# Performance work log

Measured on AMD Instinct MI355X. Metric: run time of the kernel, lower is better.

Reference implementation:

```python
import jax, jax.numpy as jnp
import numpy as np
from jax import lax

S = 2                      # window half-size (matches init_kwargs s)
K = 2 * S + 1              # kernel size = 5
SZ = float(K ** 3)         # number of voxels in the window
EPS = 1e-10


def _box_sum(x):
    """Replicate-pad then valid 3D box-sum with an all-ones K^3 kernel.
    x: [N, 1, D, H, W] -> [N, 1, D, H, W]. Same math as F.pad(mode='replicate')
    followed by Conv3d(ones kernel, valid)."""
    xp = jnp.pad(x, ((0, 0), (0, 0), (S, S), (S, S), (S, S)), mode='edge')
    kern = jnp.ones((1, 1, K, K, K), dtype=x.dtype)
    return lax.conv_general_dilated(
        xp, kern, window_strides=(1, 1, 1), padding='VALID',
        dimension_numbers=('NCDHW', 'OIDHW', 'NCDHW'))


def setup_inputs() -> dict:
    key = jax.random.key(0)
    k1, k2 = jax.random.split(key)
    shape = (2, 1, 160, 160, 160)
    im_fixed = jax.random.normal(k1, shape, dtype=jnp.float32)
    im_moving = jax.random.normal(k2, shape, dtype=jnp.float32)
    mask = jnp.ones(shape, dtype=jnp.float32)
    return {"im_fixed": im_fixed, "im_moving": im_moving, "mask": mask}


def reference(im_fixed, im_moving, mask):
    # local means
    u_F = _box_sum(im_fixed) / SZ
    u_M = _box_sum(im_moving) / SZ
    # local variances (box-sum of squared centered values, then / SZ)
    sigma_F = jnp.sqrt(_box_sum((im_fixed - u_F) ** 2) / SZ)
    sigma_M = jnp.sqrt(_box_sum((im_moving - u_M) ** 2) / SZ)
    # normalized images
    n_F = (im_fixed - u_F) / (sigma_F + EPS)
    n_M = (im_moving - u_M) / (sigma_M + EPS)
    # local cross-correlation map (box-sum, NOT divided by SZ, as in torch code)
    cross = _box_sum(n_F * n_M)
    # reduce: negative masked sum of squared LCC
    return -1.0 * jnp.sum(cross ** 2 * mask)
```

## Files before the change

### kernel.cpp

```cpp
#include <hip/hip_runtime.h>

namespace {

constexpr int LEN   = 160;
constexpr int PLANE = LEN * LEN;
constexpr int VOL   = LEN * PLANE;
constexpr float INV_SZ = 1.0f / 125.0f;
constexpr float EPS_   = 1e-10f;

constexpr int TX = 32, TY = 32, ZC = 16;
constexpr int RX = TX + 4, RY = TY + 4;
constexpr int NRAW = RX * RY;
constexpr int NCHZ = LEN / ZC;
constexpr int NBX = LEN / TX, NBY = LEN / TY;
constexpr int NXY = NBX * NBY;
constexpr int BLK  = 512;
constexpr int NWG  = NBX * NBY * NCHZ * 2;
constexpr int QW   = NWG / 8, RW = NWG % 8;

__device__ __forceinline__ int clampi(int v) {
  return v < 0 ? 0 : (v > LEN - 1 ? LEN - 1 : v);
}

struct BlkInfo { int x0, y0, z0; size_t base; };
__device__ __forceinline__ BlkInfo decodeBlock() {
  const int g = blockIdx.x + NBX * (blockIdx.y + NBY * blockIdx.z);
  const int xcd = g & 7, idx = g >> 3;
  const int w = (xcd < RW) ? xcd * (QW + 1) + idx
                           : RW * (QW + 1) + (xcd - RW) * QW + idx;
  const int half = NWG / 2;
  const int batch = w / half;
  const int rem   = w % half;
  const int zc = rem / NXY, tl = rem % NXY;
  BlkInfo bi;
  bi.x0 = (tl % NBX) * TX;
  bi.y0 = (tl / NBX) * TY;
  bi.z0 = zc * ZC;
  bi.base = (size_t)batch * VOL;
  return bi;
}

__global__ __launch_bounds__(BLK) void fuseAB(const float* __restrict__ inA,
                                              const float* __restrict__ inB,
                                              float* __restrict__ outP) {
  __shared__ __align__(16) float raw[2][2][RY][RX];
  __shared__ __align__(16) float xs [4][2][RY][RX];

  const int tid = threadIdx.x;
  const BlkInfo bi = decodeBlock();
  const int x0 = bi.x0, y0 = bi.y0, z0 = bi.z0;
  const size_t base = bi.base;

  int off[3], lly[3], llx[3];
  bool act[3];
#pragma unroll
  for (int j = 0; j < 3; ++j) {
    int i = tid + j * BLK;
    act[j] = i < NRAW;
    int ii = act[j] ? i : 0;
    lly[j] = ii / RX; llx[j] = ii % RX;
    off[j] = clampi(y0 - 2 + lly[j]) * LEN + clampi(x0 - 2 + llx[j]);
  }

  const int ly  = tid >> 4;
  const int lx0 = (tid & 15) * 2;

  float pA[2][3], pB[2][3];
  float2 rzF[6], rzM[6], rzF2[6], rzM2[6];
  float2 cnF[4], cnM[4];

  auto loadPair = [&](int t) {
#pragma unroll
    for (int p = 0; p < 2; ++p) {
      const size_t pb = base + (size_t)clampi(t + p) * PLANE;
#pragma unroll
      for (int j = 0; j < 3; ++j)
        if (act[j]) { pA[p][j] = inA[pb + off[j]]; pB[p][j] = inB[pb + off[j]]; }
    }
  };
  auto depositPair = [&]() {
#pragma unroll
    for (int p = 0; p < 2; ++p)
#pragma unroll
      for (int j = 0; j < 3; ++j)
        if (act[j]) {
          raw[0][p][lly[j]][llx[j]] = pA[p][j];
          raw[1][p][lly[j]][llx[j]] = pB[p][j];
        }
  };

  auto xsumTask = [&](int tt) {
    const int f = tt & 1, c = (tt >> 1) & 7, r = tt >> 4;
#pragma unroll
    for (int p = 0; p < 2; ++p) {
      const float* rp = &raw[f][p][r][4 * c];
      const float4 u = *(const float4*)rp;
      const float4 v = *(const float4*)(rp + 4);
      const float m = u.y + u.z + u.w;
      float4 s;
      s.x = m + u.x + v.x;
      s.y = m + v.x + v.y;
      s.z = s.y - u.y + v.z;
      s.w = s.z - u.z + v.w;
      *(float4*)&xs[f][p][r][4 * c] = s;
      float4 uq, vq;
      uq.x = u.x * u.x; uq.y = u.y * u.y; uq.z = u.z * u.z; uq.w = u.w * u.w;
      vq.x = v.x * v.x; vq.y = v.y * v.y; vq.z = v.z * v.z; vq.w = v.w * v.w;
      const float mq = uq.y + uq.z + uq.w;
      float4 q;
      q.x = mq + uq.x + vq.x;
      q.y = mq + vq.x + vq.y;
      q.z = q.y - uq.y + vq.z;
      q.w = q.z - uq.z + vq.w;
      *(float4*)&xs[2 + f][p][r][4 * c] = q;
    }
  };

  loadPair(z0 - 2);
  depositPair();
  __syncthreads();

  for (int t = z0 - 2; t <= z0 + ZC; t += 2) {
    if (t + 2 <= z0 + ZC) loadPair(t + 2);

    xsumTask(tid);
    if (tid < 576 - BLK) xsumTask(tid + BLK);

    cnF[0] = cnF[2]; cnF[1] = cnF[3]; cnM[0] = cnM[2]; cnM[1] = cnM[3];
    cnF[2] = *(const float2*)&raw[0][0][ly + 2][lx0 + 2];
    cnF[3] = *(const float2*)&raw[0][1][ly + 2][lx0 + 2];
    cnM[2] = *(const float2*)&raw[1][0][ly + 2][lx0 + 2];
    cnM[3] = *(const float2*)&raw[1][1][ly + 2][lx0 + 2];

    __syncthreads();

    if (t + 2 <= z0 + ZC) depositPair();

#pragma unroll
    for (int s = 0; s < 4; ++s) {
      rzF[s] = rzF[s + 2]; rzM[s] = rzM[s + 2];
      rzF2[s] = rzF2[s + 2]; rzM2[s] = rzM2[s + 2];
    }
#pragma unroll
    for (int p = 0; p < 2; ++p) {
      float2 sf = {0.f, 0.f}, sm = {0.f, 0.f};
      float2 sf2 = {0.f, 0.f}, sm2 = {0.f, 0.f};
#pragma unroll
      for (int k = 0; k < 5; ++k) {
        const float2 a  = *(const float2*)&xs[0][p][ly + k][lx0];
        const float2 b  = *(const float2*)&xs[1][p][ly + k][lx0];
        const float2 a2 = *(const float2*)&xs[2][p][ly + k][lx0];
        const float2 b2 = *(const float2*)&xs[3][p][ly + k][lx0];
        sf.x += a.x;  sf.y += a.y;  sm.x += b.x;  sm.y += b.y;
        sf2.x += a2.x; sf2.y += a2.y; sm2.x += b2.x; sm2.y += b2.y;
      }
      rzF[4 + p] = sf; rzM[4 + p] = sm;
      rzF2[4 + p] = sf2; rzM2[4 + p] = sm2;
    }

    if (t >= z0 + 2) {
#pragma unroll
      for (int q = 0; q < 2; ++q) {
        const int zo = t - 2 + q;
        float2 bF = {0.f, 0.f}, bM = {0.f, 0.f};
        float2 bF2 = {0.f, 0.f}, bM2 = {0.f, 0.f};
#pragma unroll
        for (int s = 0; s < 5; ++s) {
          bF.x += rzF[q + s].x;  bF.y += rzF[q + s].y;
          bM.x += rzM[q + s].x;  bM.y += rzM[q + s].y;
          bF2.x += rzF2[q + s].x; bF2.y += rzF2[q + s].y;
          bM2.x += rzM2[q + s].x; bM2.y += rzM2[q + s].y;
        }
        const size_t g = base + (size_t)zo * PLANE + (size_t)(y0 + ly) * LEN + (x0 + lx0);
        float2 o;
        {
          const float uF = bF.x * INV_SZ, uM = bM.x * INV_SZ;
          const float vF = fmaxf(bF2.x * INV_SZ - uF * uF, 0.f);
          const float vM = fmaxf(bM2.x * INV_SZ - uM * uM, 0.f);
          o.x = ((cnF[q].x - uF) / (sqrtf(vF) + EPS_)) *
                ((cnM[q].x - uM) / (sqrtf(vM) + EPS_));
        }
        {
          const float uF = bF.y * INV_SZ, uM = bM.y * INV_SZ;
          const float vF = fmaxf(bF2.y * INV_SZ - uF * uF, 0.f);
          const float vM = fmaxf(bM2.y * INV_SZ - uM * uM, 0.f);
          o.y = ((cnF[q].y - uF) / (sqrtf(vF) + EPS_)) *
                ((cnM[q].y - uM) / (sqrtf(vM) + EPS_));
        }
        *(float2*)&outP[g] = o;
      }
    }
    __syncthreads();
  }
}

__global__ __launch_bounds__(BLK) void slab1_reduce(const float* __restrict__ p,
                                                    const float* __restrict__ mask,
                                                    float* __restrict__ out) {
  __shared__ __align__(16) float raw[2][RY][RX];
  __shared__ __align__(16) float xs [2][RY][RX];
  __shared__ float wsum[BLK / 64];

  const int tid = threadIdx.x;
  const BlkInfo bi = decodeBlock();
  const int x0 = bi.x0, y0 = bi.y0, z0 = bi.z0;
  const size_t base = bi.base;

  int off[3], lly[3], llx[3];
  bool act[3];
#pragma unroll
  for (int j = 0; j < 3; ++j) {
    int i = tid + j * BLK;
    act[j] = i < NRAW;
    int ii = act[j] ? i : 0;
    lly[j] = ii / RX; llx[j] = ii % RX;
    off[j] = clampi(y0 - 2 + lly[j]) * LEN + clampi(x0 - 2 + llx[j]);
  }
  const int ly  = tid >> 4;
  const int lx0 = (tid & 15) * 2;

  float pf[2][3];
  float2 rz[6];
  float acc = 0.f;

  auto loadPair = [&](int t) {
#pragma unroll
    for (int pp = 0; pp < 2; ++pp) {
      const size_t pb = base + (size_t)clampi(t + pp) * PLANE;
#pragma unroll
      for (int j = 0; j < 3; ++j)
        if (act[j]) pf[pp][j] = p[pb + off[j]];
    }
  };
  auto depositPair = [&]() {
#pragma unroll
    for (int pp = 0; pp < 2; ++pp)
#pragma unroll
      for (int j = 0; j < 3; ++j)
        if (act[j]) raw[pp][lly[j]][llx[j]] = pf[pp][j];
  };

  loadPair(z0 - 2);
  depositPair();
  __syncthreads();

  for (int t = z0 - 2; t <= z0 + ZC; t += 2) {
    if (t + 2 <= z0 + ZC) loadPair(t + 2);

    if (tid < 288) {
      const int c = tid & 7, r = tid >> 3;
#pragma unroll
      for (int pp = 0; pp < 2; ++pp) {
        const float* rp = &raw[pp][r][4 * c];
        const float4 u = *(const float4*)rp;
        const float4 v = *(const float4*)(rp + 4);
        const float m = u.y + u.z + u.w;
        float4 s;
        s.x = m + u.x + v.x;
        s.y = m + v.x + v.y;
        s.z = s.y - u.y + v.z;
        s.w = s.z - u.z + v.w;
        *(float4*)&xs[pp][r][4 * c] = s;
      }
    }
    __syncthreads();

    if (t + 2 <= z0 + ZC) depositPair();

#pragma unroll
    for (int s = 0; s < 4; ++s) rz[s] = rz[s + 2];
#pragma unroll
    for (int pp = 0; pp < 2; ++pp) {
      float2 s2 = {0.f, 0.f};
#pragma unroll
      for (int k = 0; k < 5; ++k) {
        const float2 a = *(const float2*)&xs[pp][ly + k][lx0];
        s2.x += a.x; s2.y += a.y;
      }
      rz[4 + pp] = s2;
    }

    if (t >= z0 + 2) {
#pragma unroll
      for (int q = 0; q < 2; ++q) {
        const int zo = t - 2 + q;
        float2 bs = {0.f, 0.f};
#pragma unroll
        for (int s = 0; s < 5; ++s) { bs.x += rz[q + s].x; bs.y += rz[q + s].y; }
        const size_t g = base + (size_t)zo * PLANE + (size_t)(y0 + ly) * LEN + (x0 + lx0);
        const float2 mk = *(const float2*)&mask[g];
        acc += bs.x * bs.x * mk.x + bs.y * bs.y * mk.y;
      }
    }
    __syncthreads();
  }

#pragma unroll
  for (int o = 32; o > 0; o >>= 1) acc += __shfl_down(acc, o, 64);
  const int lane = tid & 63, wid = tid >> 6;
  if (lane == 0) wsum[wid] = acc;
  __syncthreads();
  if (tid == 0) {
    float t = 0.f;
#pragma unroll
    for (int w = 0; w < BLK / 64; ++w) t += wsum[w];
    atomicAdd(out, -t);
  }
}

}

extern "C" void kernel_launch(void* const* d_in, const int* in_sizes, int n_in,
                              void* d_out, int out_size, void* d_ws, size_t ws_size,
                              hipStream_t stream) {
  const float* F    = (const float*)d_in[0];
  const float* M    = (const float*)d_in[1];
  const float* mask = (const float*)d_in[2];
  float* out = (float*)d_out;

  float* pB = (float*)d_ws;

  hipMemsetAsync(d_out, 0, sizeof(float), stream);

  dim3 grd(NBX, NBY, NCHZ * 2), blk(BLK);

  fuseAB<<<grd, blk, 0, stream>>>(F, M, pB);
  slab1_reduce<<<grd, blk, 0, stream>>>(pB, mask, out);
}
```

Before: 186.4 us.

## Shrink tiles to 32x16 with one voxel per thread and precomputed LDS pointers

Halves the y tile height so each 512-thread block covers 32x16 voxels, one per thread, instead of two. The grid doubles, which gives more blocks to spread over the CUs. Shared-memory x-sum buffers drop their halo columns, and the per-thread addresses for LDS deposits and x-sum tasks are computed once before the loop. The smaller tile raises the halo overhead in y (20 staged rows for 16 outputs instead of 36 for 32) and narrows global stores from float2 to scalar. The XCD remap is hardcoded to the new block count of 1000.

```diff
diff --git a/kernel.cpp b/kernel.cpp
--- a/kernel.cpp
+++ b/kernel.cpp
@@ -8,15 +8,13 @@
 constexpr float INV_SZ = 1.0f / 125.0f;
 constexpr float EPS_   = 1e-10f;
 
-constexpr int TX = 32, TY = 32, ZC = 16;
+constexpr int TX = 32, TY = 16, ZC = 16;
 constexpr int RX = TX + 4, RY = TY + 4;
 constexpr int NRAW = RX * RY;
 constexpr int NCHZ = LEN / ZC;
 constexpr int NBX = LEN / TX, NBY = LEN / TY;
 constexpr int NXY = NBX * NBY;
 constexpr int BLK  = 512;
-constexpr int NWG  = NBX * NBY * NCHZ * 2;
-constexpr int QW   = NWG / 8, RW = NWG % 8;
 
 __device__ __forceinline__ int clampi(int v) {
   return v < 0 ? 0 : (v > LEN - 1 ? LEN - 1 : v);
@@ -25,10 +23,8 @@
 struct BlkInfo { int x0, y0, z0; size_t base; };
 __device__ __forceinline__ BlkInfo decodeBlock() {
   const int g = blockIdx.x + NBX * (blockIdx.y + NBY * blockIdx.z);
-  const int xcd = g & 7, idx = g >> 3;
-  const int w = (xcd < RW) ? xcd * (QW + 1) + idx
-                           : RW * (QW + 1) + (xcd - RW) * QW + idx;
-  const int half = NWG / 2;
+  const int w = (g & 7) * 125 + (g >> 3);
+  const int half = NXY * NCHZ;
   const int batch = w / half;
   const int rem   = w % half;
   const int zc = rem / NXY, tl = rem % NXY;
@@ -44,37 +40,57 @@
                                               const float* __restrict__ inB,
                                               float* __restrict__ outP) {
   __shared__ __align__(16) float raw[2][2][RY][RX];
-  __shared__ __align__(16) float xs [4][2][RY][RX];
+  __shared__ __align__(16) float xs [4][2][RY][TX];
 
   const int tid = threadIdx.x;
   const BlkInfo bi = decodeBlock();
   const int x0 = bi.x0, y0 = bi.y0, z0 = bi.z0;
   const size_t base = bi.base;
 
-  int off[3], lly[3], llx[3];
-  bool act[3];
-#pragma unroll
-  for (int j = 0; j < 3; ++j) {
+  int off[2]; float* ldst[2][2][2];
+  bool act[2];
+#pragma unroll
+  for (int j = 0; j < 2; ++j) {
     int i = tid + j * BLK;
     act[j] = i < NRAW;
     int ii = act[j] ? i : 0;
-    lly[j] = ii / RX; llx[j] = ii % RX;
-    off[j] = clampi(y0 - 2 + lly[j]) * LEN + clampi(x0 - 2 + llx[j]);
-  }
-
-  const int ly  = tid >> 4;
-  const int lx0 = (tid & 15) * 2;
-
-  float pA[2][3], pB[2][3];
-  float2 rzF[6], rzM[6], rzF2[6], rzM2[6];
-  float2 cnF[4], cnM[4];
+    const int ry = ii / RX, rx = ii % RX;
+    off[j] = clampi(y0 - 2 + ry) * LEN + clampi(x0 - 2 + rx);
+#pragma unroll
+    for (int f = 0; f < 2; ++f)
+#pragma unroll
+      for (int p = 0; p < 2; ++p) ldst[j][f][p] = &raw[f][p][ry][rx];
+  }
+
+  const float* tsrc[2]; float* tdst[2]; int ntask = (tid < 128) ? 2 : 1;
+#pragma unroll
+  for (int k = 0; k < 2; ++k) {
+    int tt = (k == 0) ? tid : tid + BLK;
+    if (tt >= 640) tt = 0;
+    const int p = tt / 320, r1 = tt % 320;
+    const int f = r1 / 160, r2 = r1 % 160;
+    const int r = r2 / 8,  c = r2 % 8;
+    tsrc[k] = &raw[f][p][r][4 * c];
+    tdst[k] = &xs[f][p][r][4 * c];
+  }
+  if (tid >= 128) ntask = 1;
+
+  const int ly = tid >> 5, lx = tid & 31;
+  const int sOff = (y0 + ly) * LEN + (x0 + lx);
+  const float* ybase = &xs[0][0][ly][lx];
+  constexpr int AS = 2 * RY * TX;
+  constexpr int PS = RY * TX;
+
+  float pA[2][2], pB[2][2];
+  float rzF[6], rzM[6], rzF2[6], rzM2[6];
+  float cnF[4], cnM[4];
 
   auto loadPair = [&](int t) {
 #pragma unroll
     for (int p = 0; p < 2; ++p) {
       const size_t pb = base + (size_t)clampi(t + p) * PLANE;
 #pragma unroll
-      for (int j = 0; j < 3; ++j)
+      for (int j = 0; j < 2; ++j)
         if (act[j]) { pA[p][j] = inA[pb + off[j]]; pB[p][j] = inB[pb + off[j]]; }
     }
   };
@@ -82,214 +98,195 @@
 #pragma unroll
     for (int p = 0; p < 2; ++p)
 #pragma unroll
-      for (int j = 0; j < 3; ++j)
-        if (act[j]) {
-          raw[0][p][lly[j]][llx[j]] = pA[p][j];
-          raw[1][p][lly[j]][llx[j]] = pB[p][j];
+      for (int j = 0; j < 2; ++j)
+        if (act[j]) { *ldst[j][0][p] = pA[p][j]; *ldst[j][1][p] = pB[p][j]; }
+  };
+
+  auto xsumTask = [&](int k) {
+    const float4 u = *(const float4*)tsrc[k];
+    const float4 v = *(const float4*)(tsrc[k] + 4);
+    const float m = u.y + u.z + u.w;
+    float4 s;
+    s.x = m + u.x + v.x;
+    s.y = m + v.x + v.y;
+    s.z = s.y - u.y + v.z;
+    s.w = s.z - u.z + v.w;
+    *(float4*)tdst[k] = s;
+    float4 uq, vq;
+    uq.x = u.x * u.x; uq.y = u.y * u.y; uq.z = u.z * u.z; uq.w = u.w * u.w;
+    vq.x = v.x * v.x; vq.y = v.y * v.y; vq.z = v.z * v.z; vq.w = v.w * v.w;
+    const float mq = uq.y + uq.z + uq.w;
+    float4 q;
+    q.x = mq + uq.x + vq.x;
+    q.y = mq + vq.x + vq.y;
+    q.z = q.y - uq.y + vq.z;
+    q.w = q.z - uq.z + vq.w;
+    *(float4*)(tdst[k] + 2 * AS) = q;
+  };
+
+  loadPair(z0 - 2);
+  depositPair();
+  __syncthreads();
+
+  for (int t = z0 - 2; t <= z0 + ZC; t += 2) {
+    if (t + 2 <= z0 + ZC) loadPair(t + 2);
+
+    xsumTask(0);
+    if (ntask == 2) xsumTask(1);
+
+    cnF[0] = cnF[2]; cnF[1] = cnF[3]; cnM[0] = cnM[2]; cnM[1] = cnM[3];
+    cnF[2] = raw[0][0][ly + 2][lx + 2];
+    cnF[3] = raw[0][1][ly + 2][lx + 2];
+    cnM[2] = raw[1][0][ly + 2][lx + 2];
+    cnM[3] = raw[1][1][ly + 2][lx + 2];
+
+    __syncthreads();
+
+    if (t + 2 <= z0 + ZC) depositPair();
+
+#pragma unroll
+    for (int s = 0; s < 4; ++s) {
+      rzF[s] = rzF[s + 2]; rzM[s] = rzM[s + 2];
+      rzF2[s] = rzF2[s + 2]; rzM2[s] = rzM2[s + 2];
+    }
+#pragma unroll
+    for (int p = 0; p < 2; ++p) {
+      float sf = 0.f, sm = 0.f, sf2 = 0.f, sm2 = 0.f;
+#pragma unroll
+      for (int k = 0; k < 5; ++k) {
+        sf  += ybase[0 * AS + p * PS + k * TX];
+        sm  += ybase[1 * AS + p * PS + k * TX];
+        sf2 += ybase[2 * AS + p * PS + k * TX];
+        sm2 += ybase[3 * AS + p * PS + k * TX];
+      }
+      rzF[4 + p] = sf; rzM[4 + p] = sm;
+      rzF2[4 + p] = sf2; rzM2[4 + p] = sm2;
+    }
+
+    if (t >= z0 + 2) {
+#pragma unroll
+      for (int q = 0; q < 2; ++q) {
+        const int zo = t - 2 + q;
+        float bF = 0.f, bM = 0.f, bF2 = 0.f, bM2 = 0.f;
+#pragma unroll
+        for (int s = 0; s < 5; ++s) {
+          bF += rzF[q + s]; bM += rzM[q + s];
+          bF2 += rzF2[q + s]; bM2 += rzM2[q + s];
         }
-  };
-
-  auto xsumTask = [&](int tt) {
-    const int f = tt & 1, c = (tt >> 1) & 7, r = tt >> 4;
-#pragma unroll
-    for (int p = 0; p < 2; ++p) {
-      const float* rp = &raw[f][p][r][4 * c];
-      const float4 u = *(const float4*)rp;
-      const float4 v = *(const float4*)(rp + 4);
+        const float uF = bF * INV_SZ, uM = bM * INV_SZ;
+        const float vF = fmaxf(bF2 * INV_SZ - uF * uF, 0.f);
+        const float vM = fmaxf(bM2 * INV_SZ - uM * uM, 0.f);
+        const float o = ((cnF[q] - uF) / (sqrtf(vF) + EPS_)) *
+                        ((cnM[q] - uM) / (sqrtf(vM) + EPS_));
+        outP[base + (size_t)zo * PLANE + sOff] = o;
+      }
+    }
+    __syncthreads();
+  }
+}
+
+__global__ __launch_bounds__(BLK) void slab1_reduce(const float* __restrict__ p,
+                                                    const float* __restrict__ mask,
+                                                    float* __restrict__ out) {
+  __shared__ __align__(16) float raw[2][RY][RX];
+  __shared__ __align__(16) float xs [2][RY][TX];
+  __shared__ float wsum[BLK / 64];
+
+  const int tid = threadIdx.x;
+  const BlkInfo bi = decodeBlock();
+  const int x0 = bi.x0, y0 = bi.y0, z0 = bi.z0;
+  const size_t base = bi.base;
+
+  int off[2]; float* ldst[2][2];
+  bool act[2];
+#pragma unroll
+  for (int j = 0; j < 2; ++j) {
+    int i = tid + j * BLK;
+    act[j] = i < NRAW;
+    int ii = act[j] ? i : 0;
+    const int ry = ii / RX, rx = ii % RX;
+    off[j] = clampi(y0 - 2 + ry) * LEN + clampi(x0 - 2 + rx);
+#pragma unroll
+    for (int pp = 0; pp < 2; ++pp) ldst[j][pp] = &raw[pp][ry][rx];
+  }
+
+  const bool tact = tid < 320;
+  const float* tsrc; float* tdst;
+  {
+    int tt = tact ? tid : 0;
+    const int pp = tt / 160, r1 = tt % 160;
+    const int r = r1 / 8, c = r1 % 8;
+    tsrc = &raw[pp][r][4 * c];
+    tdst = &xs[pp][r][4 * c];
+  }
+
+  const int ly = tid >> 5, lx = tid & 31;
+  const int sOff = (y0 + ly) * LEN + (x0 + lx);
+  const float* ybase = &xs[0][ly][lx];
+  constexpr int PS = RY * TX;
+
+  float pf[2][2];
+  float rz[6];
+  float acc = 0.f;
+
+  auto loadPair = [&](int t) {
+#pragma unroll
+    for (int pp = 0; pp < 2; ++pp) {
+      const size_t pb = base + (size_t)clampi(t + pp) * PLANE;
+#pragma unroll
+      for (int j = 0; j < 2; ++j)
+        if (act[j]) pf[pp][j] = p[pb + off[j]];
+    }
+  };
+  auto depositPair = [&]() {
+#pragma unroll
+    for (int pp = 0; pp < 2; ++pp)
+#pragma unroll
+      for (int j = 0; j < 2; ++j)
+        if (act[j]) *ldst[j][pp] = pf[pp][j];
+  };
+
+  loadPair(z0 - 2);
+  depositPair();
+  __syncthreads();
+
+  for (int t = z0 - 2; t <= z0 + ZC; t += 2) {
+    if (t + 2 <= z0 + ZC) loadPair(t + 2);
+
+    if (tact) {
+      const float4 u = *(const float4*)tsrc;
+      const float4 v = *(const float4*)(tsrc + 4);
       const float m = u.y + u.z + u.w;
       float4 s;
       s.x = m + u.x + v.x;
       s.y = m + v.x + v.y;
       s.z = s.y - u.y + v.z;
       s.w = s.z - u.z + v.w;
-      *(float4*)&xs[f][p][r][4 * c] = s;
-      float4 uq, vq;
-      uq.x = u.x * u.x; uq.y = u.y * u.y; uq.z = u.z * u.z; uq.w = u.w * u.w;
-      vq.x = v.x * v.x; vq.y = v.y * v.y; vq.z = v.z * v.z; vq.w = v.w * v.w;
-      const float mq = uq.y + uq.z + uq.w;
-      float4 q;
-      q.x = mq + uq.x + vq.x;
-      q.y = mq + vq.x + vq.y;
-      q.z = q.y - uq.y + vq.z;
-      q.w = q.z - uq.z + vq.w;
-      *(float4*)&xs[2 + f][p][r][4 * c] = q;
-    }
-  };
-
-  loadPair(z0 - 2);
-  depositPair();
-  __syncthreads();
-
-  for (int t = z0 - 2; t <= z0 + ZC; t += 2) {
-    if (t + 2 <= z0 + ZC) loadPair(t + 2);
-
-    xsumTask(tid);
-    if (tid < 576 - BLK) xsumTask(tid + BLK);
-
-    cnF[0] = cnF[2]; cnF[1] = cnF[3]; cnM[0] = cnM[2]; cnM[1] = cnM[3];
-    cnF[2] = *(const float2*)&raw[0][0][ly + 2][lx0 + 2];
-    cnF[3] = *(const float2*)&raw[0][1][ly + 2][lx0 + 2];
-    cnM[2] = *(const float2*)&raw[1][0][ly + 2][lx0 + 2];
-    cnM[3] = *(const float2*)&raw[1][1][ly + 2][lx0 + 2];
-
+      *(float4*)tdst = s;
+    }
     __syncthreads();
 
     if (t + 2 <= z0 + ZC) depositPair();
 
 #pragma unroll
-    for (int s = 0; s < 4; ++s) {
-      rzF[s] = rzF[s + 2]; rzM[s] = rzM[s + 2];
-      rzF2[s] = rzF2[s + 2]; rzM2[s] = rzM2[s + 2];
-    }
-#pragma unroll
-    for (int p = 0; p < 2; ++p) {
-      float2 sf = {0.f, 0.f}, sm = {0.f, 0.f};
-      float2 sf2 = {0.f, 0.f}, sm2 = {0.f, 0.f};
-#pragma unroll
-      for (int k = 0; k < 5; ++k) {
-        const float2 a  = *(const float2*)&xs[0][p][ly + k][lx0];
-        const float2 b  = *(const float2*)&xs[1][p][ly + k][lx0];
-        const float2 a2 = *(const float2*)&xs[2][p][ly + k][lx0];
-        const float2 b2 = *(const float2*)&xs[3][p][ly + k][lx0];
-        sf.x += a.x;  sf.y += a.y;  sm.x += b.x;  sm.y += b.y;
-        sf2.x += a2.x; sf2.y += a2.y; sm2.x += b2.x; sm2.y += b2.y;
-      }
-      rzF[4 + p] = sf; rzM[4 + p] = sm;
-      rzF2[4 + p] = sf2; rzM2[4 + p] = sm2;
+    for (int s = 0; s < 4; ++s) rz[s] = rz[s + 2];
+#pragma unroll
+    for (int pp = 0; pp < 2; ++pp) {
+      float s2 = 0.f;
+#pragma unroll
+      for (int k = 0; k < 5; ++k) s2 += ybase[pp * PS + k * TX];
+      rz[4 + pp] = s2;
     }
 
     if (t >= z0 + 2) {
 #pragma unroll
       for (int q = 0; q < 2; ++q) {
         const int zo = t - 2 + q;
-        float2 bF = {0.f, 0.f}, bM = {0.f, 0.f};
-        float2 bF2 = {0.f, 0.f}, bM2 = {0.f, 0.f};
-#pragma unroll
-        for (int s = 0; s < 5; ++s) {
-          bF.x += rzF[q + s].x;  bF.y += rzF[q + s].y;
-          bM.x += rzM[q + s].x;  bM.y += rzM[q + s].y;
-          bF2.x += rzF2[q + s].x; bF2.y += rzF2[q + s].y;
-          bM2.x += rzM2[q + s].x; bM2.y += rzM2[q + s].y;
-        }
-        const size_t g = base + (size_t)zo * PLANE + (size_t)(y0 + ly) * LEN + (x0 + lx0);
-        float2 o;
-        {
-          const float uF = bF.x * INV_SZ, uM = bM.x * INV_SZ;
-          const float vF = fmaxf(bF2.x * INV_SZ - uF * uF, 0.f);
-          const float vM = fmaxf(bM2.x * INV_SZ - uM * uM, 0.f);
-          o.x = ((cnF[q].x - uF) / (sqrtf(vF) + EPS_)) *
-                ((cnM[q].x - uM) / (sqrtf(vM) + EPS_));
-        }
-        {
-          const float uF = bF.y * INV_SZ, uM = bM.y * INV_SZ;
-          const float vF = fmaxf(bF2.y * INV_SZ - uF * uF, 0.f);
-          const float vM = fmaxf(bM2.y * INV_SZ - uM * uM, 0.f);
-          o.y = ((cnF[q].y - uF) / (sqrtf(vF) + EPS_)) *
-                ((cnM[q].y - uM) / (sqrtf(vM) + EPS_));
-        }
-        *(float2*)&outP[g] = o;
-      }
-    }
-    __syncthreads();
-  }
-}
-
-__global__ __launch_bounds__(BLK) void slab1_reduce(const float* __restrict__ p,
-                                                    const float* __restrict__ mask,
-                                                    float* __restrict__ out) {
-  __shared__ __align__(16) float raw[2][RY][RX];
-  __shared__ __align__(16) float xs [2][RY][RX];
-  __shared__ float wsum[BLK / 64];
-
-  const int tid = threadIdx.x;
-  const BlkInfo bi = decodeBlock();
-  const int x0 = bi.x0, y0 = bi.y0, z0 = bi.z0;
-  const size_t base = bi.base;
-
-  int off[3], lly[3], llx[3];
-  bool act[3];
-#pragma unroll
-  for (int j = 0; j < 3; ++j) {
-    int i = tid + j * BLK;
-    act[j] = i < NRAW;
-    int ii = act[j] ? i : 0;
-    lly[j] = ii / RX; llx[j] = ii % RX;
-    off[j] = clampi(y0 - 2 + lly[j]) * LEN + clampi(x0 - 2 + llx[j]);
-  }
-  const int ly  = tid >> 4;
-  const int lx0 = (tid & 15) * 2;
-
-  float pf[2][3];
-  float2 rz[6];
-  float acc = 0.f;
-
-  auto loadPair = [&](int t) {
-#pragma unroll
-    for (int pp = 0; pp < 2; ++pp) {
-      const size_t pb = base + (size_t)clampi(t + pp) * PLANE;
-#pragma unroll
-      for (int j = 0; j < 3; ++j)
-        if (act[j]) pf[pp][j] = p[pb + off[j]];
-    }
-  };
-  auto depositPair = [&]() {
-#pragma unroll
-    for (int pp = 0; pp < 2; ++pp)
-#pragma unroll
-      for (int j = 0; j < 3; ++j)
-        if (act[j]) raw[pp][lly[j]][llx[j]] = pf[pp][j];
-  };
-
-  loadPair(z0 - 2);
-  depositPair();
-  __syncthreads();
-
-  for (int t = z0 - 2; t <= z0 + ZC; t += 2) {
-    if (t + 2 <= z0 + ZC) loadPair(t + 2);
-
-    if (tid < 288) {
-      const int c = tid & 7, r = tid >> 3;
-#pragma unroll
-      for (int pp = 0; pp < 2; ++pp) {
-        const float* rp = &raw[pp][r][4 * c];
-        const float4 u = *(const float4*)rp;
-        const float4 v = *(const float4*)(rp + 4);
-        const float m = u.y + u.z + u.w;
-        float4 s;
-        s.x = m + u.x + v.x;
-        s.y = m + v.x + v.y;
-        s.z = s.y - u.y + v.z;
-        s.w = s.z - u.z + v.w;
-        *(float4*)&xs[pp][r][4 * c] = s;
-      }
-    }
-    __syncthreads();
-
-    if (t + 2 <= z0 + ZC) depositPair();
-
-#pragma unroll
-    for (int s = 0; s < 4; ++s) rz[s] = rz[s + 2];
-#pragma unroll
-    for (int pp = 0; pp < 2; ++pp) {
-      float2 s2 = {0.f, 0.f};
-#pragma unroll
-      for (int k = 0; k < 5; ++k) {
-        const float2 a = *(const float2*)&xs[pp][ly + k][lx0];
-        s2.x += a.x; s2.y += a.y;
-      }
-      rz[4 + pp] = s2;
-    }
-
-    if (t >= z0 + 2) {
-#pragma unroll
-      for (int q = 0; q < 2; ++q) {
-        const int zo = t - 2 + q;
-        float2 bs = {0.f, 0.f};
-#pragma unroll
-        for (int s = 0; s < 5; ++s) { bs.x += rz[q + s].x; bs.y += rz[q + s].y; }
-        const size_t g = base + (size_t)zo * PLANE + (size_t)(y0 + ly) * LEN + (x0 + lx0);
-        const float2 mk = *(const float2*)&mask[g];
-        acc += bs.x * bs.x * mk.x + bs.y * bs.y * mk.y;
+        float bs = 0.f;
+#pragma unroll
+        for (int s = 0; s < 5; ++s) bs += rz[q + s];
+        const size_t g = base + (size_t)zo * PLANE + sOff;
+        acc += bs * bs * mask[g];
       }
     }
     __syncthreads();
@@ -301,10 +298,10 @@
   if (lane == 0) wsum[wid] = acc;
   __syncthreads();
   if (tid == 0) {
-    float t = 0.f;
-#pragma unroll
-    for (int w = 0; w < BLK / 64; ++w) t += wsum[w];
-    atomicAdd(out, -t);
+    float tt = 0.f;
+#pragma unroll
+    for (int w = 0; w < BLK / 64; ++w) tt += wsum[w];
+    atomicAdd(out, -tt);
   }
 }
 
```

Measured after the change: 178.4 us. -4.3%, faster.

## Retile fuseAB to 32x16x32 blocks with precomputed LDS pointers

Applied to the files above, without the earlier changes.

The first kernel now uses a 32x16 xy tile with a 32-deep z chunk, down from 32x32x16. The longer z chunk spreads the z halo over more output planes, and the smaller xy footprint cuts halo loads and LDS size. Shared-memory source and destination pointers are precomputed once, and the normalization uses one division instead of two. The catch is that only 256 of 512 threads do the output stage, which halves per-thread compute parallelism in that phase. The block count per kernel stays at 500.

```diff
diff --git a/kernel.cpp b/kernel.cpp
--- a/kernel.cpp
+++ b/kernel.cpp
@@ -8,64 +8,79 @@
 constexpr float INV_SZ = 1.0f / 125.0f;
 constexpr float EPS_   = 1e-10f;
 
-constexpr int TX = 32, TY = 32, ZC = 16;
-constexpr int RX = TX + 4, RY = TY + 4;
-constexpr int NRAW = RX * RY;
-constexpr int NCHZ = LEN / ZC;
-constexpr int NBX = LEN / TX, NBY = LEN / TY;
-constexpr int NXY = NBX * NBY;
-constexpr int BLK  = 512;
-constexpr int NWG  = NBX * NBY * NCHZ * 2;
-constexpr int QW   = NWG / 8, RW = NWG % 8;
+constexpr int BLK = 512;
+
+constexpr int FTX = 32, FTY = 16, FZC = 32;
+constexpr int FRX = FTX + 4, FRY = FTY + 4;
+constexpr int FNRAW = FRX * FRY;
+constexpr int FNBX = 5, FNBY = 10, FNXY = 50, FNCHZ = 5;
+
+constexpr int STX = 32, STY = 32, SZC = 16;
+constexpr int SRX = STX + 4, SRY = STY + 4;
+constexpr int SNRAW = SRX * SRY;
+constexpr int SNBX = 5, SNBY = 5, SNXY = 25, SNCHZ = 10;
+
+constexpr int NWG = 500, QW = 62, RW = 4;
 
 __device__ __forceinline__ int clampi(int v) {
   return v < 0 ? 0 : (v > LEN - 1 ? LEN - 1 : v);
 }
 
-struct BlkInfo { int x0, y0, z0; size_t base; };
-__device__ __forceinline__ BlkInfo decodeBlock() {
-  const int g = blockIdx.x + NBX * (blockIdx.y + NBY * blockIdx.z);
+__device__ __forceinline__ int swz(int g) {
   const int xcd = g & 7, idx = g >> 3;
-  const int w = (xcd < RW) ? xcd * (QW + 1) + idx
-                           : RW * (QW + 1) + (xcd - RW) * QW + idx;
-  const int half = NWG / 2;
-  const int batch = w / half;
-  const int rem   = w % half;
-  const int zc = rem / NXY, tl = rem % NXY;
-  BlkInfo bi;
-  bi.x0 = (tl % NBX) * TX;
-  bi.y0 = (tl / NBX) * TY;
-  bi.z0 = zc * ZC;
-  bi.base = (size_t)batch * VOL;
-  return bi;
+  return (xcd < RW) ? xcd * (QW + 1) + idx
+                    : RW * (QW + 1) + (xcd - RW) * QW + idx;
 }
 
 __global__ __launch_bounds__(BLK) void fuseAB(const float* __restrict__ inA,
                                               const float* __restrict__ inB,
                                               float* __restrict__ outP) {
-  __shared__ __align__(16) float raw[2][2][RY][RX];
-  __shared__ __align__(16) float xs [4][2][RY][RX];
+  __shared__ __align__(16) float raw[2][2][FRY][FRX];
+  __shared__ __align__(16) float xs [4][2][FRY][FTX];
 
   const int tid = threadIdx.x;
-  const BlkInfo bi = decodeBlock();
-  const int x0 = bi.x0, y0 = bi.y0, z0 = bi.z0;
-  const size_t base = bi.base;
-
-  int off[3], lly[3], llx[3];
-  bool act[3];
-#pragma unroll
-  for (int j = 0; j < 3; ++j) {
+  const int g = blockIdx.x + FNBX * (blockIdx.y + FNBY * blockIdx.z);
+  const int w = swz(g);
+  const int batch = w / 250, rem = w % 250;
+  const int zc = rem / FNXY, tl = rem % FNXY;
+  const int x0 = (tl % FNBX) * FTX;
+  const int y0 = (tl / FNBX) * FTY;
+  const int z0 = zc * FZC;
+  const size_t base = (size_t)batch * VOL;
+
+  int off[2]; float* ldst[2][2][2];
+  bool act[2];
+#pragma unroll
+  for (int j = 0; j < 2; ++j) {
     int i = tid + j * BLK;
-    act[j] = i < NRAW;
+    act[j] = i < FNRAW;
     int ii = act[j] ? i : 0;
-    lly[j] = ii / RX; llx[j] = ii % RX;
-    off[j] = clampi(y0 - 2 + lly[j]) * LEN + clampi(x0 - 2 + llx[j]);
-  }
-
+    const int ry = ii / FRX, rx = ii % FRX;
+    off[j] = clampi(y0 - 2 + ry) * LEN + clampi(x0 - 2 + rx);
+#pragma unroll
+    for (int f = 0; f < 2; ++f)
+#pragma unroll
+      for (int p = 0; p < 2; ++p) ldst[j][f][p] = &raw[f][p][ry][rx];
+  }
+
+  const float* tsrc[2]; float* tdst[2];
+#pragma unroll
+  for (int k = 0; k < 2; ++k) {
+    int tt = (k == 0) ? tid : tid + BLK;
+    if (tt >= 640) tt = 0;
+    const int p = tt / 320, r1 = tt % 320;
+    const int f = r1 / 160, r2 = r1 % 160;
+    const int r = r2 / 8,  c = r2 % 8;
+    tsrc[k] = &raw[f][p][r][4 * c];
+    tdst[k] = &xs[f][p][r][4 * c];
+  }
+
+  const bool qact = tid < 256;
   const int ly  = tid >> 4;
   const int lx0 = (tid & 15) * 2;
-
-  float pA[2][3], pB[2][3];
+  const int sOff = (y0 + ly) * LEN + (x0 + lx0);
+
+  float pA[2][2], pB[2][2];
   float2 rzF[6], rzM[6], rzF2[6], rzM2[6];
   float2 cnF[4], cnM[4];
 
@@ -74,7 +89,7 @@
     for (int p = 0; p < 2; ++p) {
       const size_t pb = base + (size_t)clampi(t + p) * PLANE;
 #pragma unroll
-      for (int j = 0; j < 3; ++j)
+      for (int j = 0; j < 2; ++j)
         if (act[j]) { pA[p][j] = inA[pb + off[j]]; pB[p][j] = inB[pb + off[j]]; }
     }
   };
@@ -82,112 +97,107 @@
 #pragma unroll
     for (int p = 0; p < 2; ++p)
 #pragma unroll
-      for (int j = 0; j < 3; ++j)
-        if (act[j]) {
-          raw[0][p][lly[j]][llx[j]] = pA[p][j];
-          raw[1][p][lly[j]][llx[j]] = pB[p][j];
-        }
-  };
-
-  auto xsumTask = [&](int tt) {
-    const int f = tt & 1, c = (tt >> 1) & 7, r = tt >> 4;
-#pragma unroll
-    for (int p = 0; p < 2; ++p) {
-      const float* rp = &raw[f][p][r][4 * c];
-      const float4 u = *(const float4*)rp;
-      const float4 v = *(const float4*)(rp + 4);
-      const float m = u.y + u.z + u.w;
-      float4 s;
-      s.x = m + u.x + v.x;
-      s.y = m + v.x + v.y;
-      s.z = s.y - u.y + v.z;
-      s.w = s.z - u.z + v.w;
-      *(float4*)&xs[f][p][r][4 * c] = s;
-      float4 uq, vq;
-      uq.x = u.x * u.x; uq.y = u.y * u.y; uq.z = u.z * u.z; uq.w = u.w * u.w;
-      vq.x = v.x * v.x; vq.y = v.y * v.y; vq.z = v.z * v.z; vq.w = v.w * v.w;
-      const float mq = uq.y + uq.z + uq.w;
-      float4 q;
-      q.x = mq + uq.x + vq.x;
-      q.y = mq + vq.x + vq.y;
-      q.z = q.y - uq.y + vq.z;
-      q.w = q.z - uq.z + vq.w;
-      *(float4*)&xs[2 + f][p][r][4 * c] = q;
-    }
+      for (int j = 0; j < 2; ++j)
+        if (act[j]) { *ldst[j][0][p] = pA[p][j]; *ldst[j][1][p] = pB[p][j]; }
+  };
+
+  auto xsumTask = [&](int k) {
+    const float4 u = *(const float4*)tsrc[k];
+    const float4 v = *(const float4*)(tsrc[k] + 4);
+    const float m = u.y + u.z + u.w;
+    float4 s;
+    s.x = m + u.x + v.x;
+    s.y = m + v.x + v.y;
+    s.z = s.y - u.y + v.z;
+    s.w = s.z - u.z + v.w;
+    *(float4*)tdst[k] = s;
+    float4 uq, vq;
+    uq.x = u.x * u.x; uq.y = u.y * u.y; uq.z = u.z * u.z; uq.w = u.w * u.w;
+    vq.x = v.x * v.x; vq.y = v.y * v.y; vq.z = v.z * v.z; vq.w = v.w * v.w;
+    const float mq = uq.y + uq.z + uq.w;
+    float4 q;
+    q.x = mq + uq.x + vq.x;
+    q.y = mq + vq.x + vq.y;
+    q.z = q.y - uq.y + vq.z;
+    q.w = q.z - uq.z + vq.w;
+    *(float4*)(tdst[k] + 2 * 2 * FRY * FTX) = q;
   };
 
   loadPair(z0 - 2);
   depositPair();
   __syncthreads();
 
-  for (int t = z0 - 2; t <= z0 + ZC; t += 2) {
-    if (t + 2 <= z0 + ZC) loadPair(t + 2);
-
-    xsumTask(tid);
-    if (tid < 576 - BLK) xsumTask(tid + BLK);
-
-    cnF[0] = cnF[2]; cnF[1] = cnF[3]; cnM[0] = cnM[2]; cnM[1] = cnM[3];
-    cnF[2] = *(const float2*)&raw[0][0][ly + 2][lx0 + 2];
-    cnF[3] = *(const float2*)&raw[0][1][ly + 2][lx0 + 2];
-    cnM[2] = *(const float2*)&raw[1][0][ly + 2][lx0 + 2];
-    cnM[3] = *(const float2*)&raw[1][1][ly + 2][lx0 + 2];
+  for (int t = z0 - 2; t <= z0 + FZC; t += 2) {
+    if (t + 2 <= z0 + FZC) loadPair(t + 2);
+
+    xsumTask(0);
+    if (tid < 128) xsumTask(1);
+
+    if (qact) {
+      cnF[0] = cnF[2]; cnF[1] = cnF[3]; cnM[0] = cnM[2]; cnM[1] = cnM[3];
+      cnF[2] = *(const float2*)&raw[0][0][ly + 2][lx0 + 2];
+      cnF[3] = *(const float2*)&raw[0][1][ly + 2][lx0 + 2];
+      cnM[2] = *(const float2*)&raw[1][0][ly + 2][lx0 + 2];
+      cnM[3] = *(const float2*)&raw[1][1][ly + 2][lx0 + 2];
+    }
 
     __syncthreads();
 
-    if (t + 2 <= z0 + ZC) depositPair();
-
-#pragma unroll
-    for (int s = 0; s < 4; ++s) {
-      rzF[s] = rzF[s + 2]; rzM[s] = rzM[s + 2];
-      rzF2[s] = rzF2[s + 2]; rzM2[s] = rzM2[s + 2];
-    }
-#pragma unroll
-    for (int p = 0; p < 2; ++p) {
-      float2 sf = {0.f, 0.f}, sm = {0.f, 0.f};
-      float2 sf2 = {0.f, 0.f}, sm2 = {0.f, 0.f};
-#pragma unroll
-      for (int k = 0; k < 5; ++k) {
-        const float2 a  = *(const float2*)&xs[0][p][ly + k][lx0];
-        const float2 b  = *(const float2*)&xs[1][p][ly + k][lx0];
-        const float2 a2 = *(const float2*)&xs[2][p][ly + k][lx0];
-        const float2 b2 = *(const float2*)&xs[3][p][ly + k][lx0];
-        sf.x += a.x;  sf.y += a.y;  sm.x += b.x;  sm.y += b.y;
-        sf2.x += a2.x; sf2.y += a2.y; sm2.x += b2.x; sm2.y += b2.y;
-      }
-      rzF[4 + p] = sf; rzM[4 + p] = sm;
-      rzF2[4 + p] = sf2; rzM2[4 + p] = sm2;
-    }
-
-    if (t >= z0 + 2) {
-#pragma unroll
-      for (int q = 0; q < 2; ++q) {
-        const int zo = t - 2 + q;
-        float2 bF = {0.f, 0.f}, bM = {0.f, 0.f};
-        float2 bF2 = {0.f, 0.f}, bM2 = {0.f, 0.f};
-#pragma unroll
-        for (int s = 0; s < 5; ++s) {
-          bF.x += rzF[q + s].x;  bF.y += rzF[q + s].y;
-          bM.x += rzM[q + s].x;  bM.y += rzM[q + s].y;
-          bF2.x += rzF2[q + s].x; bF2.y += rzF2[q + s].y;
-          bM2.x += rzM2[q + s].x; bM2.y += rzM2[q + s].y;
+    if (t + 2 <= z0 + FZC) depositPair();
+
+    if (qact) {
+#pragma unroll
+      for (int s = 0; s < 4; ++s) {
+        rzF[s] = rzF[s + 2]; rzM[s] = rzM[s + 2];
+        rzF2[s] = rzF2[s + 2]; rzM2[s] = rzM2[s + 2];
+      }
+#pragma unroll
+      for (int p = 0; p < 2; ++p) {
+        float2 sf = {0.f, 0.f}, sm = {0.f, 0.f};
+        float2 sf2 = {0.f, 0.f}, sm2 = {0.f, 0.f};
+#pragma unroll
+        for (int k = 0; k < 5; ++k) {
+          const float2 a  = *(const float2*)&xs[0][p][ly + k][lx0];
+          const float2 b  = *(const float2*)&xs[1][p][ly + k][lx0];
+          const float2 a2 = *(const float2*)&xs[2][p][ly + k][lx0];
+          const float2 b2 = *(const float2*)&xs[3][p][ly + k][lx0];
+          sf.x += a.x;   sf.y += a.y;   sm.x += b.x;   sm.y += b.y;
+          sf2.x += a2.x; sf2.y += a2.y; sm2.x += b2.x; sm2.y += b2.y;
         }
-        const size_t g = base + (size_t)zo * PLANE + (size_t)(y0 + ly) * LEN + (x0 + lx0);
-        float2 o;
-        {
-          const float uF = bF.x * INV_SZ, uM = bM.x * INV_SZ;
-          const float vF = fmaxf(bF2.x * INV_SZ - uF * uF, 0.f);
-          const float vM = fmaxf(bM2.x * INV_SZ - uM * uM, 0.f);
-          o.x = ((cnF[q].x - uF) / (sqrtf(vF) + EPS_)) *
-                ((cnM[q].x - uM) / (sqrtf(vM) + EPS_));
+        rzF[4 + p] = sf; rzM[4 + p] = sm;
+        rzF2[4 + p] = sf2; rzM2[4 + p] = sm2;
+      }
+
+      if (t >= z0 + 2) {
+#pragma unroll
+        for (int q = 0; q < 2; ++q) {
+          const int zo = t - 2 + q;
+          float2 bF = {0.f, 0.f}, bM = {0.f, 0.f};
+          float2 bF2 = {0.f, 0.f}, bM2 = {0.f, 0.f};
+#pragma unroll
+          for (int s = 0; s < 5; ++s) {
+            bF.x += rzF[q + s].x;   bF.y += rzF[q + s].y;
+            bM.x += rzM[q + s].x;   bM.y += rzM[q + s].y;
+            bF2.x += rzF2[q + s].x; bF2.y += rzF2[q + s].y;
+            bM2.x += rzM2[q + s].x; bM2.y += rzM2[q + s].y;
+          }
+          float2 o;
+          {
+            const float uF = bF.x * INV_SZ, uM = bM.x * INV_SZ;
+            const float vF = fmaxf(bF2.x * INV_SZ - uF * uF, 0.f);
+            const float vM = fmaxf(bM2.x * INV_SZ - uM * uM, 0.f);
+            o.x = ((cnF[q].x - uF) * (cnM[q].x - uM)) /
+                  ((sqrtf(vF) + EPS_) * (sqrtf(vM) + EPS_));
+          }
+          {
+            const float uF = bF.y * INV_SZ, uM = bM.y * INV_SZ;
+            const float vF = fmaxf(bF2.y * INV_SZ - uF * uF, 0.f);
+            const float vM = fmaxf(bM2.y * INV_SZ - uM * uM, 0.f);
+            o.y = ((cnF[q].y - uF) * (cnM[q].y - uM)) /
+                  ((sqrtf(vF) + EPS_) * (sqrtf(vM) + EPS_));
+          }
+          *(float2*)&outP[base + (size_t)zo * PLANE + sOff] = o;
         }
-        {
-          const float uF = bF.y * INV_SZ, uM = bM.y * INV_SZ;
-          const float vF = fmaxf(bF2.y * INV_SZ - uF * uF, 0.f);
-          const float vM = fmaxf(bM2.y * INV_SZ - uM * uM, 0.f);
-          o.y = ((cnF[q].y - uF) / (sqrtf(vF) + EPS_)) *
-                ((cnM[q].y - uM) / (sqrtf(vM) + EPS_));
-        }
-        *(float2*)&outP[g] = o;
       }
     }
     __syncthreads();
@@ -197,23 +207,28 @@
 __global__ __launch_bounds__(BLK) void slab1_reduce(const float* __restrict__ p,
                                                     const float* __restrict__ mask,
                                                     float* __restrict__ out) {
-  __shared__ __align__(16) float raw[2][RY][RX];
-  __shared__ __align__(16) float xs [2][RY][RX];
+  __shared__ __align__(16) float raw[2][SRY][SRX];
+  __shared__ __align__(16) float xs [2][SRY][SRX];
   __shared__ float wsum[BLK / 64];
 
   const int tid = threadIdx.x;
-  const BlkInfo bi = decodeBlock();
-  const int x0 = bi.x0, y0 = bi.y0, z0 = bi.z0;
-  const size_t base = bi.base;
+  const int g = blockIdx.x + SNBX * (blockIdx.y + SNBY * blockIdx.z);
+  const int w = swz(g);
+  const int batch = w / 250, rem = w % 250;
+  const int zc = rem / SNXY, tl = rem % SNXY;
+  const int x0 = (tl % SNBX) * STX;
+  const int y0 = (tl / SNBX) * STY;
+  const int z0 = zc * SZC;
+  const size_t base = (size_t)batch * VOL;
 
   int off[3], lly[3], llx[3];
   bool act[3];
 #pragma unroll
   for (int j = 0; j < 3; ++j) {
     int i = tid + j * BLK;
-    act[j] = i < NRAW;
+    act[j] = i < SNRAW;
     int ii = act[j] ? i : 0;
-    lly[j] = ii / RX; llx[j] = ii % RX;
+    lly[j] = ii / SRX; llx[j] = ii % SRX;
     off[j] = clampi(y0 - 2 + lly[j]) * LEN + clampi(x0 - 2 + llx[j]);
   }
   const int ly  = tid >> 4;
@@ -244,8 +259,8 @@
   depositPair();
   __syncthreads();
 
-  for (int t = z0 - 2; t <= z0 + ZC; t += 2) {
-    if (t + 2 <= z0 + ZC) loadPair(t + 2);
+  for (int t = z0 - 2; t <= z0 + SZC; t += 2) {
+    if (t + 2 <= z0 + SZC) loadPair(t + 2);
 
     if (tid < 288) {
       const int c = tid & 7, r = tid >> 3;
@@ -265,7 +280,7 @@
     }
     __syncthreads();
 
-    if (t + 2 <= z0 + ZC) depositPair();
+    if (t + 2 <= z0 + SZC) depositPair();
 
 #pragma unroll
     for (int s = 0; s < 4; ++s) rz[s] = rz[s + 2];
@@ -287,8 +302,8 @@
         float2 bs = {0.f, 0.f};
 #pragma unroll
         for (int s = 0; s < 5; ++s) { bs.x += rz[q + s].x; bs.y += rz[q + s].y; }
-        const size_t g = base + (size_t)zo * PLANE + (size_t)(y0 + ly) * LEN + (x0 + lx0);
-        const float2 mk = *(const float2*)&mask[g];
+        const size_t gg = base + (size_t)zo * PLANE + (size_t)(y0 + ly) * LEN + (x0 + lx0);
+        const float2 mk = *(const float2*)&mask[gg];
         acc += bs.x * bs.x * mk.x + bs.y * bs.y * mk.y;
       }
     }
@@ -301,10 +316,10 @@
   if (lane == 0) wsum[wid] = acc;
   __syncthreads();
   if (tid == 0) {
-    float t = 0.f;
-#pragma unroll
-    for (int w = 0; w < BLK / 64; ++w) t += wsum[w];
-    atomicAdd(out, -t);
+    float tt = 0.f;
+#pragma unroll
+    for (int ww = 0; ww < BLK / 64; ++ww) tt += wsum[ww];
+    atomicAdd(out, -tt);
   }
 }
 
@@ -322,8 +337,9 @@
 
   hipMemsetAsync(d_out, 0, sizeof(float), stream);
 
-  dim3 grd(NBX, NBY, NCHZ * 2), blk(BLK);
-
-  fuseAB<<<grd, blk, 0, stream>>>(F, M, pB);
-  slab1_reduce<<<grd, blk, 0, stream>>>(pB, mask, out);
-}
+  dim3 gf(FNBX, FNBY, FNCHZ * 2), blk(BLK);
+  dim3 gs(SNBX, SNBY, SNCHZ * 2);
+
+  fuseAB<<<gf, blk, 0, stream>>>(F, M, pB);
+  slab1_reduce<<<gs, blk, 0, stream>>>(pB, mask, out);
+}
```

Measured after the change: 163.3 us. -12.4%, faster.
